# Optimization experiments

Hardware: AMD Instinct MI355X
Metric: run time of the kernel (lower is better)

## Reference

```python
import jax, jax.numpy as jnp
import numpy as np

CUTOFF_ENDS = [0, 20000, 40000, 200000, 267735]
D_EMBS = [1024, 256, 64, 16]
D_PROJ = 1024
EMB_SCALE = 1.0  # scale_emb=False


def setup_inputs() -> dict:
    key = jax.random.key(0)
    ks = jax.random.split(key, 9)
    out = {"inp": jax.random.randint(ks[0], (8, 2048), 0, CUTOFF_ENDS[-1], dtype=jnp.int64)
           if jax.config.jax_enable_x64 else
           jax.random.randint(ks[0], (8, 2048), 0, CUTOFF_ENDS[-1], dtype=jnp.int32)}
    for i in range(4):
        n_i = CUTOFF_ENDS[i + 1] - CUTOFF_ENDS[i]
        out[f"emb{i}"] = jax.random.normal(ks[1 + i], (n_i, D_EMBS[i]), jnp.float32) * 0.02
        out[f"proj{i}"] = jax.random.normal(ks[5 + i], (D_PROJ, D_EMBS[i]), jnp.float32) * 0.02
    return out


def reference(inp, emb0, emb1, emb2, emb3, proj0, proj1, proj2, proj3):
    # Faithful to AdaptiveEmbedding.forward: per-cutoff mask -> embedding lookup
    # -> linear projection (F.linear with weight [d_proj, d_emb_i]) -> scatter-back.
    # Instead of data-dependent nonzero/index_copy (not jit-able), each bucket
    # computes over all tokens with in-bucket indices clipped, then masked-adds;
    # disjoint buckets make this mathematically identical to the scatter.
    embs = [emb0, emb1, emb2, emb3]
    projs = [proj0, proj1, proj2, proj3]
    flat = inp.reshape(-1)                      # [N]
    out = jnp.zeros((flat.shape[0], D_PROJ), jnp.float32)
    for i in range(4):
        l, r = CUTOFF_ENDS[i], CUTOFF_ENDS[i + 1]
        mask = (flat >= l) & (flat < r)         # [N]
        idx = jnp.clip(flat - l, 0, r - l - 1)  # in-bucket ids, clipped for safety
        e = embs[i][idx]                        # [N, d_i] gather
        p = e @ projs[i].T                      # [N, d_proj] projection
        out = out + jnp.where(mask[:, None], p, 0.0)
    out = out.reshape(*inp.shape, D_PROJ)
    return out * EMB_SCALE if EMB_SCALE != 1.0 else out
```

## Files before the change

### kernel.cpp

```cpp
#include <hip/hip_runtime.h>

#define DPROJ 1024

typedef short  bf16x8 __attribute__((ext_vector_type(8)));
typedef float  f32x4  __attribute__((ext_vector_type(4)));
typedef unsigned short u16x4 __attribute__((ext_vector_type(4)));

__device__ __forceinline__ unsigned short f2bf(float f) {
  unsigned u = __builtin_bit_cast(unsigned, f);
  u += 0x7FFFu + ((u >> 16) & 1u);
  return (unsigned short)(u >> 16);
}

__device__ __forceinline__ int bucket_of(int v) {
  return (v < 0) ? -1 : (v >= 200000) ? 3 : (v >= 40000) ? 2 : (v >= 20000) ? 1 : 0;
}

__global__ __launch_bounds__(256) void count_kernel(const int* __restrict__ inp, int n,
                                                    int* __restrict__ blkcnt) {
  int t = blockIdx.x * 256 + threadIdx.x;
  int lane = threadIdx.x & 63, w = threadIdx.x >> 6;
  int v = (t < n) ? inp[t] : -1;
  int b = bucket_of(v);
  __shared__ int cnt[4][4];
#pragma unroll
  for (int i = 0; i < 4; ++i) {
    unsigned long long m = __ballot(b == i);
    if (lane == 0) cnt[w][i] = __popcll(m);
  }
  __syncthreads();
  if (threadIdx.x < 4) {
    int s = cnt[0][threadIdx.x] + cnt[1][threadIdx.x] +
            cnt[2][threadIdx.x] + cnt[3][threadIdx.x];
    blkcnt[blockIdx.x * 4 + threadIdx.x] = s;
  }
}

__global__ __launch_bounds__(256) void scatter_kernel(const int* __restrict__ inp, int n,
                                                      const int* __restrict__ blkcnt, int nb,
                                                      unsigned* __restrict__ lists,
                                                      int* __restrict__ counts) {
  int t = blockIdx.x * 256 + threadIdx.x;
  int lane = threadIdx.x & 63, w = threadIdx.x >> 6;
  __shared__ int cnt[4][4];
  __shared__ int off_s[4];
  {
    int sv = (lane < nb) ? blkcnt[lane * 4 + w] : 0;
    int x = sv;
#pragma unroll
    for (int d = 1; d < 64; d <<= 1) {
      int y = __shfl_up(x, d);
      if (lane >= d) x += y;
    }
    int myoff = __shfl(x - sv, blockIdx.x);
    if (lane == 0) off_s[w] = myoff;
    if (blockIdx.x == 0 && lane == 63) counts[w] = x;
  }
  int v = (t < n) ? inp[t] : -1;
  int b = bucket_of(v);
  int lo = (b == 3) ? 200000 : (b == 2) ? 40000 : (b == 1) ? 20000 : 0;
  int myrank = 0;
#pragma unroll
  for (int i = 0; i < 4; ++i) {
    unsigned long long m = __ballot(b == i);
    if (lane == 0) cnt[w][i] = __popcll(m);
    if (b == i) myrank = __popcll(m & ((1ull << lane) - 1ull));
  }
  __syncthreads();
  if (b >= 0) {
    int prefix = 0;
    for (int w2 = 0; w2 < w; ++w2) prefix += cnt[w2][b];
    int pos = off_s[b] + prefix + myrank;
    lists[(size_t)b * n + pos] = ((unsigned)(v - lo) << 14) | (unsigned)t;
  }
}

template <int D>
__device__ __forceinline__ void gemm_heavy(const float* __restrict__ emb,
                                           const float* __restrict__ proj,
                                           const unsigned* __restrict__ list,
                                           int cnt, int r0, int c0,
                                           float* __restrict__ out, char* smem) {
  constexpr int NCH = D / 64;
  const int tid  = threadIdx.x;
  const int lane = tid & 63;
  const int w    = tid >> 6;
  const int wr   = w >> 1, wc = w & 1;
  const int lr   = lane & 15, t16 = lane >> 4;

  char* Ab = smem;
  char* Bb = smem + 8192;
  unsigned* toks = (unsigned*)(smem + 24576);

  if (tid < 64) {
    int p = r0 + tid;
    toks[tid] = (p < cnt) ? list[p] : 0u;
  }
  __syncthreads();

  int ra[4], ca[4], cb[8], c4b[8];
#pragma unroll
  for (int i = 0; i < 4; ++i) {
    int q = tid + i * 256;
    ra[i] = q >> 4; ca[i] = (q & 15) * 4;
  }
#pragma unroll
  for (int i = 0; i < 8; ++i) {
    int q = tid + i * 256;
    cb[i] = q >> 4; c4b[i] = (q & 15) * 4;
  }
  const float* abase[4];
#pragma unroll
  for (int i = 0; i < 4; ++i)
    abase[i] = emb + (size_t)(toks[ra[i]] >> 14) * D + ca[i];
  const float* bbase[8];
#pragma unroll
  for (int i = 0; i < 8; ++i)
    bbase[i] = proj + (size_t)(c0 + cb[i]) * D + c4b[i];

  float4 arg[4], brg[8];
#pragma unroll
  for (int i = 0; i < 4; ++i) arg[i] = *reinterpret_cast<const float4*>(abase[i]);
#pragma unroll
  for (int i = 0; i < 8; ++i) brg[i] = *reinterpret_cast<const float4*>(bbase[i]);

  f32x4 acc[2][4];
#pragma unroll
  for (int fi = 0; fi < 2; ++fi)
#pragma unroll
    for (int fj = 0; fj < 4; ++fj) acc[fi][fj] = (f32x4){0.f, 0.f, 0.f, 0.f};

  for (int ch = 0; ch < NCH; ++ch) {
#pragma unroll
    for (int i = 0; i < 4; ++i) {
      u16x4 o = {f2bf(arg[i].x), f2bf(arg[i].y), f2bf(arg[i].z), f2bf(arg[i].w)};
      *reinterpret_cast<u16x4*>(Ab + ra[i] * 128 + ((ca[i] * 2) ^ ((ra[i] & 7) << 4))) = o;
    }
#pragma unroll
    for (int i = 0; i < 8; ++i) {
      u16x4 o = {f2bf(brg[i].x), f2bf(brg[i].y), f2bf(brg[i].z), f2bf(brg[i].w)};
      *reinterpret_cast<u16x4*>(Bb + cb[i] * 128 + ((c4b[i] * 2) ^ ((cb[i] & 7) << 4))) = o;
    }
    __syncthreads();

    if (ch + 1 < NCH) {
      const int k1 = (ch + 1) * 64;
#pragma unroll
      for (int i = 0; i < 4; ++i) arg[i] = *reinterpret_cast<const float4*>(abase[i] + k1);
#pragma unroll
      for (int i = 0; i < 8; ++i) brg[i] = *reinterpret_cast<const float4*>(bbase[i] + k1);
    }

#pragma unroll
    for (int s = 0; s < 2; ++s) {
      bf16x8 a[2], b[4];
#pragma unroll
      for (int fi = 0; fi < 2; ++fi) {
        int row = wr * 32 + fi * 16 + lr;
        a[fi] = *reinterpret_cast<const bf16x8*>(
            Ab + row * 128 + ((s * 64 + t16 * 16) ^ ((row & 7) << 4)));
      }
#pragma unroll
      for (int fj = 0; fj < 4; ++fj) {
        int col = wc * 64 + fj * 16 + lr;
        b[fj] = *reinterpret_cast<const bf16x8*>(
            Bb + col * 128 + ((s * 64 + t16 * 16) ^ ((col & 7) << 4)));
      }
#pragma unroll
      for (int fi = 0; fi < 2; ++fi)
#pragma unroll
        for (int fj = 0; fj < 4; ++fj)
          acc[fi][fj] = __builtin_amdgcn_mfma_f32_16x16x32_bf16(a[fi], b[fj], acc[fi][fj], 0, 0, 0);
    }
    __syncthreads();
  }

  float* T = reinterpret_cast<float*>(smem + w * 4352);
#pragma unroll
  for (int fi = 0; fi < 2; ++fi) {
#pragma unroll
    for (int fj = 0; fj < 4; ++fj)
#pragma unroll
      for (int reg = 0; reg < 4; ++reg)
        T[(t16 * 4 + reg) * 68 + fj * 16 + lr] = acc[fi][fj][reg];
#pragma unroll
    for (int rr = 0; rr < 4; ++rr) {
      int p = wr * 32 + fi * 16 + rr * 4 + t16;
      if (r0 + p < cnt) {
        float4 v = *reinterpret_cast<const float4*>(&T[(rr * 4 + t16) * 68 + lr * 4]);
        *reinterpret_cast<float4*>(out + (size_t)(toks[p] & 16383u) * DPROJ +
                                   c0 + wc * 64 + lr * 4) = v;
      }
    }
  }
}

template <int D>
__device__ __forceinline__ void gemm_light(const float* __restrict__ emb,
                                           const float* __restrict__ proj,
                                           const unsigned* __restrict__ list,
                                           int cnt, int r0, int c0,
                                           float* __restrict__ out, char* smem) {
  constexpr int S = (D == 64) ? 2 : 1;
  const int tid  = threadIdx.x;
  const int lane = tid & 63;
  const int w    = tid >> 6;
  const int wr   = w >> 1, wc = w & 1;
  const int lr   = lane & 15, t16 = lane >> 4;

  unsigned* toks = (unsigned*)smem;
  if (tid < 64) {
    int p = r0 + tid;
    toks[tid] = (p < cnt) ? list[p] : 0u;
  }
  __syncthreads();

  bf16x8 a[2][S], b[4][S];
#pragma unroll
  for (int fi = 0; fi < 2; ++fi) {
    const float* eb = emb + (size_t)(toks[wr * 32 + fi * 16 + lr] >> 14) * D;
#pragma unroll
    for (int s = 0; s < S; ++s) {
      float4 lo = make_float4(0.f, 0.f, 0.f, 0.f), hi = lo;
      if (D == 64 || t16 < 2) {
        lo = *reinterpret_cast<const float4*>(eb + s * 32 + t16 * 8);
        hi = *reinterpret_cast<const float4*>(eb + s * 32 + t16 * 8 + 4);
      }
      bf16x8 r;
      r[0] = (short)f2bf(lo.x); r[1] = (short)f2bf(lo.y);
      r[2] = (short)f2bf(lo.z); r[3] = (short)f2bf(lo.w);
      r[4] = (short)f2bf(hi.x); r[5] = (short)f2bf(hi.y);
      r[6] = (short)f2bf(hi.z); r[7] = (short)f2bf(hi.w);
      a[fi][s] = r;
    }
  }
#pragma unroll
  for (int fj = 0; fj < 4; ++fj) {
    const float* pb = proj + (size_t)(c0 + wc * 64 + fj * 16 + lr) * D;
#pragma unroll
    for (int s = 0; s < S; ++s) {
      float4 lo = make_float4(0.f, 0.f, 0.f, 0.f), hi = lo;
      if (D == 64 || t16 < 2) {
        lo = *reinterpret_cast<const float4*>(pb + s * 32 + t16 * 8);
        hi = *reinterpret_cast<const float4*>(pb + s * 32 + t16 * 8 + 4);
      }
      bf16x8 r;
      r[0] = (short)f2bf(lo.x); r[1] = (short)f2bf(lo.y);
      r[2] = (short)f2bf(lo.z); r[3] = (short)f2bf(lo.w);
      r[4] = (short)f2bf(hi.x); r[5] = (short)f2bf(hi.y);
      r[6] = (short)f2bf(hi.z); r[7] = (short)f2bf(hi.w);
      b[fj][s] = r;
    }
  }

  f32x4 acc[2][4];
#pragma unroll
  for (int fi = 0; fi < 2; ++fi)
#pragma unroll
    for (int fj = 0; fj < 4; ++fj) acc[fi][fj] = (f32x4){0.f, 0.f, 0.f, 0.f};
#pragma unroll
  for (int s = 0; s < S; ++s)
#pragma unroll
    for (int fi = 0; fi < 2; ++fi)
#pragma unroll
      for (int fj = 0; fj < 4; ++fj)
        acc[fi][fj] = __builtin_amdgcn_mfma_f32_16x16x32_bf16(a[fi][s], b[fj][s], acc[fi][fj], 0, 0, 0);

  float* T = reinterpret_cast<float*>(smem + 256) + w * 1088;
#pragma unroll
  for (int fi = 0; fi < 2; ++fi) {
#pragma unroll
    for (int fj = 0; fj < 4; ++fj)
#pragma unroll
      for (int reg = 0; reg < 4; ++reg)
        T[(t16 * 4 + reg) * 68 + fj * 16 + lr] = acc[fi][fj][reg];
#pragma unroll
    for (int rr = 0; rr < 4; ++rr) {
      int p = wr * 32 + fi * 16 + rr * 4 + t16;
      if (r0 + p < cnt) {
        float4 v = *reinterpret_cast<const float4*>(&T[(rr * 4 + t16) * 68 + lr * 4]);
        *reinterpret_cast<float4*>(out + (size_t)(toks[p] & 16383u) * DPROJ +
                                   c0 + wc * 64 + lr * 4) = v;
      }
    }
  }
}

__global__ __launch_bounds__(256) void gemm_all(
    const float* __restrict__ e0, const float* __restrict__ p0,
    const float* __restrict__ e1, const float* __restrict__ p1,
    const float* __restrict__ e2, const float* __restrict__ p2,
    const float* __restrict__ e3, const float* __restrict__ p3,
    const int* __restrict__ counts, const unsigned* __restrict__ lists,
    float* __restrict__ out, int n) {
  extern __shared__ char smem[];
  int bx = blockIdx.x;
  int t  = bx >> 3;
  int c0 = (bx & 7) * 128;
  int4 c = *reinterpret_cast<const int4*>(counts);
  int t0 = (c.x + 63) >> 6, t1 = (c.y + 63) >> 6,
      t2 = (c.z + 63) >> 6, t3 = (c.w + 63) >> 6;
  if (t < t0) { gemm_heavy<1024>(e0, p0, lists,               c.x, t * 64, c0, out, smem); return; }
  t -= t0;
  if (t < t1) { gemm_heavy< 256>(e1, p1, lists + (size_t)n,   c.y, t * 64, c0, out, smem); return; }
  t -= t1;
  if (t < t2) { gemm_light<64>(e2, p2, lists + (size_t)2 * n, c.z, t * 64, c0, out, smem); return; }
  t -= t2;
  if (t < t3) { gemm_light<16>(e3, p3, lists + (size_t)3 * n, c.w, t * 64, c0, out, smem); return; }
}

extern "C" void kernel_launch(void* const* d_in, const int* in_sizes, int n_in,
                              void* d_out, int out_size, void* d_ws, size_t ws_size,
                              hipStream_t stream) {
  const int*   inp   = (const int*)d_in[0];
  const float* emb0  = (const float*)d_in[1];
  const float* proj0 = (const float*)d_in[2];
  const float* emb1  = (const float*)d_in[3];
  const float* proj1 = (const float*)d_in[4];
  const float* emb2  = (const float*)d_in[5];
  const float* proj2 = (const float*)d_in[6];
  const float* emb3  = (const float*)d_in[7];
  const float* proj3 = (const float*)d_in[8];
  float* out = (float*)d_out;
  const int n = in_sizes[0];

  int*      counts = (int*)d_ws;
  int*      blkcnt = (int*)d_ws + 4;
  unsigned* lists  = (unsigned*)d_ws + 260;

  const int nb = (n + 255) / 256;
  count_kernel<<<dim3(nb), dim3(256), 0, stream>>>(inp, n, blkcnt);
  scatter_kernel<<<dim3(nb), dim3(256), 0, stream>>>(inp, n, blkcnt, nb, lists, counts);

  dim3 grid(259 * 8, 1, 1);
  size_t smem_bytes = 24576 + 64 * sizeof(unsigned);
  gemm_all<<<grid, dim3(256), smem_bytes, stream>>>(emb0, proj0, emb1, proj1,
                                                    emb2, proj2, emb3, proj3,
                                                    counts, lists, out, n);
}
```

Baseline: 43.82 us.

## Pre-convert projections to bf16, split-K the heavy bucket, double-buffer loads

Adds a pre-pass that converts all projection matrices to bf16 in workspace, fused with the bucket counting kernel, so GEMM blocks read half-width B tiles without per-block conversion. The heavy bucket 0 (D=1024) is split four ways along K for up to `cap` tiles. Each split writes partials to workspace, and a new reduce kernel sums them and scatters rows into the output. The heavy GEMM loop is fully unrolled with two register sets of prefetched loads. The goal is better load balance, since bucket-0 blocks were long-running stragglers, and lower conversion cost. The price is an extra launch, partial-sum memory traffic, a projection conversion on every call, and higher register pressure.

```diff
diff --git a/kernel.cpp b/kernel.cpp
--- a/kernel.cpp
+++ b/kernel.cpp
@@ -4,7 +4,6 @@
 
 typedef short  bf16x8 __attribute__((ext_vector_type(8)));
 typedef float  f32x4  __attribute__((ext_vector_type(4)));
-typedef unsigned short u16x4 __attribute__((ext_vector_type(4)));
 
 __device__ __forceinline__ unsigned short f2bf(float f) {
   unsigned u = __builtin_bit_cast(unsigned, f);
@@ -12,27 +11,52 @@
   return (unsigned short)(u >> 16);
 }
 
+__device__ __forceinline__ bf16x8 pack8(float4 lo, float4 hi) {
+  bf16x8 r;
+  r[0] = (short)f2bf(lo.x); r[1] = (short)f2bf(lo.y);
+  r[2] = (short)f2bf(lo.z); r[3] = (short)f2bf(lo.w);
+  r[4] = (short)f2bf(hi.x); r[5] = (short)f2bf(hi.y);
+  r[6] = (short)f2bf(hi.z); r[7] = (short)f2bf(hi.w);
+  return r;
+}
+
 __device__ __forceinline__ int bucket_of(int v) {
-  return (v < 0) ? -1 : (v >= 200000) ? 3 : (v >= 40000) ? 2 : (v >= 20000) ? 1 : 0;
-}
-
-__global__ __launch_bounds__(256) void count_kernel(const int* __restrict__ inp, int n,
-                                                    int* __restrict__ blkcnt) {
-  int t = blockIdx.x * 256 + threadIdx.x;
-  int lane = threadIdx.x & 63, w = threadIdx.x >> 6;
-  int v = (t < n) ? inp[t] : -1;
-  int b = bucket_of(v);
-  __shared__ int cnt[4][4];
-#pragma unroll
-  for (int i = 0; i < 4; ++i) {
-    unsigned long long m = __ballot(b == i);
-    if (lane == 0) cnt[w][i] = __popcll(m);
-  }
-  __syncthreads();
-  if (threadIdx.x < 4) {
-    int s = cnt[0][threadIdx.x] + cnt[1][threadIdx.x] +
-            cnt[2][threadIdx.x] + cnt[3][threadIdx.x];
-    blkcnt[blockIdx.x * 4 + threadIdx.x] = s;
+  return (v >= 200000) ? 3 : (v >= 40000) ? 2 : (v >= 20000) ? 1 : 0;
+}
+
+__global__ __launch_bounds__(256) void convert_count(
+    const float* __restrict__ p0, const float* __restrict__ p1,
+    const float* __restrict__ p2, const float* __restrict__ p3,
+    unsigned short* __restrict__ pb,
+    const int* __restrict__ inp, int n, int nb, int* __restrict__ blkcnt) {
+  size_t base = ((size_t)blockIdx.x * 256 + threadIdx.x) * 8;
+  if (base < 1392640u) {
+    const float* src;
+    if      (base < 1048576u) src = p0 + base;
+    else if (base < 1310720u) src = p1 + (base - 1048576u);
+    else if (base < 1376256u) src = p2 + (base - 1310720u);
+    else                      src = p3 + (base - 1376256u);
+    float4 lo = reinterpret_cast<const float4*>(src)[0];
+    float4 hi = reinterpret_cast<const float4*>(src)[1];
+    *reinterpret_cast<bf16x8*>(pb + base) = pack8(lo, hi);
+  }
+  if (blockIdx.x < (unsigned)nb) {
+    int t = blockIdx.x * 256 + threadIdx.x;
+    int lane = threadIdx.x & 63, w = threadIdx.x >> 6;
+    int v = (t < n) ? inp[t] : -1;
+    int b = (v < 0) ? -1 : bucket_of(v);
+    __shared__ int cnt[4][4];
+#pragma unroll
+    for (int i = 0; i < 4; ++i) {
+      unsigned long long m = __ballot(b == i);
+      if (lane == 0) cnt[w][i] = __popcll(m);
+    }
+    __syncthreads();
+    if (threadIdx.x < 4) {
+      int s = cnt[0][threadIdx.x] + cnt[1][threadIdx.x] +
+              cnt[2][threadIdx.x] + cnt[3][threadIdx.x];
+      blkcnt[blockIdx.x * 4 + threadIdx.x] = s;
+    }
   }
 }
 
@@ -57,7 +81,7 @@
     if (blockIdx.x == 0 && lane == 63) counts[w] = x;
   }
   int v = (t < n) ? inp[t] : -1;
-  int b = bucket_of(v);
+  int b = (v < 0) ? -1 : bucket_of(v);
   int lo = (b == 3) ? 200000 : (b == 2) ? 40000 : (b == 1) ? 20000 : 0;
   int myrank = 0;
 #pragma unroll
@@ -75,13 +99,12 @@
   }
 }
 
-template <int D>
+template <int D, int CHB, bool PARTIAL>
 __device__ __forceinline__ void gemm_heavy(const float* __restrict__ emb,
-                                           const float* __restrict__ proj,
+                                           const unsigned short* __restrict__ pbD,
                                            const unsigned* __restrict__ list,
-                                           int cnt, int r0, int c0,
-                                           float* __restrict__ out, char* smem) {
-  constexpr int NCH = D / 64;
+                                           int cnt, int r0, int c0, int ch0,
+                                           float* __restrict__ dst, char* smem) {
   const int tid  = threadIdx.x;
   const int lane = tid & 63;
   const int w    = tid >> 6;
@@ -98,31 +121,43 @@
   }
   __syncthreads();
 
-  int ra[4], ca[4], cb[8], c4b[8];
+  int rowA[2], kkA[2], colB[4], kkB[4];
+#pragma unroll
+  for (int i = 0; i < 2; ++i) {
+    int g = tid + i * 256;
+    rowA[i] = g >> 3; kkA[i] = (g & 7) * 8;
+  }
 #pragma unroll
   for (int i = 0; i < 4; ++i) {
-    int q = tid + i * 256;
-    ra[i] = q >> 4; ca[i] = (q & 15) * 4;
-  }
-#pragma unroll
-  for (int i = 0; i < 8; ++i) {
-    int q = tid + i * 256;
-    cb[i] = q >> 4; c4b[i] = (q & 15) * 4;
-  }
-  const float* abase[4];
+    int g = tid + i * 256;
+    colB[i] = g >> 3; kkB[i] = (g & 7) * 8;
+  }
+  const float* abase[2];
+#pragma unroll
+  for (int i = 0; i < 2; ++i)
+    abase[i] = emb + (size_t)(toks[rowA[i]] >> 14) * D + kkA[i];
+  const unsigned short* bbase[4];
 #pragma unroll
   for (int i = 0; i < 4; ++i)
-    abase[i] = emb + (size_t)(toks[ra[i]] >> 14) * D + ca[i];
-  const float* bbase[8];
-#pragma unroll
-  for (int i = 0; i < 8; ++i)
-    bbase[i] = proj + (size_t)(c0 + cb[i]) * D + c4b[i];
-
-  float4 arg[4], brg[8];
-#pragma unroll
-  for (int i = 0; i < 4; ++i) arg[i] = *reinterpret_cast<const float4*>(abase[i]);
-#pragma unroll
-  for (int i = 0; i < 8; ++i) brg[i] = *reinterpret_cast<const float4*>(bbase[i]);
+    bbase[i] = pbD + (size_t)(c0 + colB[i]) * D + kkB[i];
+
+  float4  arg[2][2][2];
+  bf16x8  brg[2][4];
+
+#define LOAD_SET(S_, K0_)                                                   \
+  {                                                                         \
+    _Pragma("unroll")                                                       \
+    for (int i = 0; i < 2; ++i) {                                           \
+      arg[S_][i][0] = *reinterpret_cast<const float4*>(abase[i] + (K0_));   \
+      arg[S_][i][1] = *reinterpret_cast<const float4*>(abase[i] + (K0_) + 4);\
+    }                                                                       \
+    _Pragma("unroll")                                                       \
+    for (int i = 0; i < 4; ++i)                                             \
+      brg[S_][i] = *reinterpret_cast<const bf16x8*>(bbase[i] + (K0_));      \
+  }
+
+  LOAD_SET(0, ch0 * 64)
+  if (CHB > 1) LOAD_SET(1, (ch0 + 1) * 64)
 
   f32x4 acc[2][4];
 #pragma unroll
@@ -130,26 +165,22 @@
 #pragma unroll
     for (int fj = 0; fj < 4; ++fj) acc[fi][fj] = (f32x4){0.f, 0.f, 0.f, 0.f};
 
-  for (int ch = 0; ch < NCH; ++ch) {
-#pragma unroll
-    for (int i = 0; i < 4; ++i) {
-      u16x4 o = {f2bf(arg[i].x), f2bf(arg[i].y), f2bf(arg[i].z), f2bf(arg[i].w)};
-      *reinterpret_cast<u16x4*>(Ab + ra[i] * 128 + ((ca[i] * 2) ^ ((ra[i] & 7) << 4))) = o;
-    }
-#pragma unroll
-    for (int i = 0; i < 8; ++i) {
-      u16x4 o = {f2bf(brg[i].x), f2bf(brg[i].y), f2bf(brg[i].z), f2bf(brg[i].w)};
-      *reinterpret_cast<u16x4*>(Bb + cb[i] * 128 + ((c4b[i] * 2) ^ ((cb[i] & 7) << 4))) = o;
-    }
+#pragma unroll
+  for (int ch = 0; ch < CHB; ++ch) {
+    const int cur = ch & 1;
+#pragma unroll
+    for (int i = 0; i < 2; ++i) {
+      bf16x8 o = pack8(arg[cur][i][0], arg[cur][i][1]);
+      *reinterpret_cast<bf16x8*>(Ab + rowA[i] * 128 +
+                                 ((kkA[i] * 2) ^ ((rowA[i] & 7) << 4))) = o;
+    }
+#pragma unroll
+    for (int i = 0; i < 4; ++i)
+      *reinterpret_cast<bf16x8*>(Bb + colB[i] * 128 +
+                                 ((kkB[i] * 2) ^ ((colB[i] & 7) << 4))) = brg[cur][i];
     __syncthreads();
 
-    if (ch + 1 < NCH) {
-      const int k1 = (ch + 1) * 64;
-#pragma unroll
-      for (int i = 0; i < 4; ++i) arg[i] = *reinterpret_cast<const float4*>(abase[i] + k1);
-#pragma unroll
-      for (int i = 0; i < 8; ++i) brg[i] = *reinterpret_cast<const float4*>(bbase[i] + k1);
-    }
+    if (ch + 2 < CHB) LOAD_SET(cur, (ch0 + ch + 2) * 64)
 
 #pragma unroll
     for (int s = 0; s < 2; ++s) {
@@ -174,6 +205,7 @@
     }
     __syncthreads();
   }
+#undef LOAD_SET
 
   float* T = reinterpret_cast<float*>(smem + w * 4352);
 #pragma unroll
@@ -188,8 +220,11 @@
       int p = wr * 32 + fi * 16 + rr * 4 + t16;
       if (r0 + p < cnt) {
         float4 v = *reinterpret_cast<const float4*>(&T[(rr * 4 + t16) * 68 + lr * 4]);
-        *reinterpret_cast<float4*>(out + (size_t)(toks[p] & 16383u) * DPROJ +
-                                   c0 + wc * 64 + lr * 4) = v;
+        if (PARTIAL)
+          *reinterpret_cast<float4*>(dst + (size_t)p * 128 + wc * 64 + lr * 4) = v;
+        else
+          *reinterpret_cast<float4*>(dst + (size_t)(toks[p] & 16383u) * DPROJ +
+                                     c0 + wc * 64 + lr * 4) = v;
       }
     }
   }
@@ -197,7 +232,7 @@
 
 template <int D>
 __device__ __forceinline__ void gemm_light(const float* __restrict__ emb,
-                                           const float* __restrict__ proj,
+                                           const unsigned short* __restrict__ pbD,
                                            const unsigned* __restrict__ list,
                                            int cnt, int r0, int c0,
                                            float* __restrict__ out, char* smem) {
@@ -226,30 +261,18 @@
         lo = *reinterpret_cast<const float4*>(eb + s * 32 + t16 * 8);
         hi = *reinterpret_cast<const float4*>(eb + s * 32 + t16 * 8 + 4);
       }
-      bf16x8 r;
-      r[0] = (short)f2bf(lo.x); r[1] = (short)f2bf(lo.y);
-      r[2] = (short)f2bf(lo.z); r[3] = (short)f2bf(lo.w);
-      r[4] = (short)f2bf(hi.x); r[5] = (short)f2bf(hi.y);
-      r[6] = (short)f2bf(hi.z); r[7] = (short)f2bf(hi.w);
-      a[fi][s] = r;
+      a[fi][s] = pack8(lo, hi);
     }
   }
 #pragma unroll
   for (int fj = 0; fj < 4; ++fj) {
-    const float* pb = proj + (size_t)(c0 + wc * 64 + fj * 16 + lr) * D;
+    const unsigned short* pbc = pbD + (size_t)(c0 + wc * 64 + fj * 16 + lr) * D;
 #pragma unroll
     for (int s = 0; s < S; ++s) {
-      float4 lo = make_float4(0.f, 0.f, 0.f, 0.f), hi = lo;
-      if (D == 64 || t16 < 2) {
-        lo = *reinterpret_cast<const float4*>(pb + s * 32 + t16 * 8);
-        hi = *reinterpret_cast<const float4*>(pb + s * 32 + t16 * 8 + 4);
-      }
-      bf16x8 r;
-      r[0] = (short)f2bf(lo.x); r[1] = (short)f2bf(lo.y);
-      r[2] = (short)f2bf(lo.z); r[3] = (short)f2bf(lo.w);
-      r[4] = (short)f2bf(hi.x); r[5] = (short)f2bf(hi.y);
-      r[6] = (short)f2bf(hi.z); r[7] = (short)f2bf(hi.w);
-      b[fj][s] = r;
+      bf16x8 z = {0, 0, 0, 0, 0, 0, 0, 0};
+      if (D == 64 || t16 < 2)
+        z = *reinterpret_cast<const bf16x8*>(pbc + s * 32 + t16 * 8);
+      b[fj][s] = z;
     }
   }
 
@@ -287,26 +310,82 @@
 }
 
 __global__ __launch_bounds__(256) void gemm_all(
-    const float* __restrict__ e0, const float* __restrict__ p0,
-    const float* __restrict__ e1, const float* __restrict__ p1,
-    const float* __restrict__ e2, const float* __restrict__ p2,
-    const float* __restrict__ e3, const float* __restrict__ p3,
+    const float* __restrict__ e0, const float* __restrict__ e1,
+    const float* __restrict__ e2, const float* __restrict__ e3,
+    const unsigned short* __restrict__ pb,
     const int* __restrict__ counts, const unsigned* __restrict__ lists,
-    float* __restrict__ out, int n) {
+    float* __restrict__ part, float* __restrict__ out, int n, int cap) {
   extern __shared__ char smem[];
-  int bx = blockIdx.x;
-  int t  = bx >> 3;
-  int c0 = (bx & 7) * 128;
   int4 c = *reinterpret_cast<const int4*>(counts);
   int t0 = (c.x + 63) >> 6, t1 = (c.y + 63) >> 6,
       t2 = (c.z + 63) >> 6, t3 = (c.w + 63) >> 6;
-  if (t < t0) { gemm_heavy<1024>(e0, p0, lists,               c.x, t * 64, c0, out, smem); return; }
-  t -= t0;
-  if (t < t1) { gemm_heavy< 256>(e1, p1, lists + (size_t)n,   c.y, t * 64, c0, out, smem); return; }
-  t -= t1;
-  if (t < t2) { gemm_light<64>(e2, p2, lists + (size_t)2 * n, c.z, t * 64, c0, out, smem); return; }
-  t -= t2;
-  if (t < t3) { gemm_light<16>(e3, p3, lists + (size_t)3 * n, c.w, t * 64, c0, out, smem); return; }
+  int sk = (t0 < cap) ? t0 : cap;
+  int y = blockIdx.x;
+  if (y < sk * 32) {
+    int nb0 = sk * 8;
+    int kz = y / nb0, r = y % nb0;
+    int tile = r >> 3, slice = r & 7;
+    float* dst = part + ((size_t)(r * 4 + kz)) * 8192;
+    gemm_heavy<1024, 4, true>(e0, pb, lists, c.x, tile * 64, slice * 128,
+                              kz * 4, dst, smem);
+    return;
+  }
+  y -= sk * 32;
+  if (y < (t0 - sk) * 8) {
+    int tile = sk + (y >> 3), slice = y & 7;
+    gemm_heavy<1024, 16, false>(e0, pb, lists, c.x, tile * 64, slice * 128,
+                                0, out, smem);
+    return;
+  }
+  y -= (t0 - sk) * 8;
+  if (y < t1 * 8) {
+    gemm_heavy<256, 4, false>(e1, pb + 1048576, lists + (size_t)n, c.y,
+                              (y >> 3) * 64, (y & 7) * 128, 0, out, smem);
+    return;
+  }
+  y -= t1 * 8;
+  if (y < t2 * 8) {
+    gemm_light<64>(e2, pb + 1310720, lists + (size_t)2 * n, c.z,
+                   (y >> 3) * 64, (y & 7) * 128, out, smem);
+    return;
+  }
+  y -= t2 * 8;
+  if (y < t3 * 8) {
+    gemm_light<16>(e3, pb + 1376256, lists + (size_t)3 * n, c.w,
+                   (y >> 3) * 64, (y & 7) * 128, out, smem);
+    return;
+  }
+}
+
+__global__ __launch_bounds__(256) void reduce_b0(const int* __restrict__ counts,
+                                                 const unsigned* __restrict__ list0,
+                                                 const float* __restrict__ part,
+                                                 float* __restrict__ out, int cap) {
+  int cnt = counts[0];
+  int tiles = (cnt + 63) >> 6;
+  if (tiles > cap) tiles = cap;
+  int tile = blockIdx.y, slice = blockIdx.x;
+  if (tile >= tiles) return;
+  const float* base = part + ((size_t)((tile * 8 + slice) * 4)) * 8192;
+  int tid = threadIdx.x;
+  int r0 = tile * 64;
+#pragma unroll
+  for (int pass = 0; pass < 8; ++pass) {
+    int row = pass * 8 + (tid >> 5);
+    int p = r0 + row;
+    if (p < cnt) {
+      int off = row * 128 + (tid & 31) * 4;
+      float4 v0 = *reinterpret_cast<const float4*>(base + off);
+      float4 v1 = *reinterpret_cast<const float4*>(base + 8192 + off);
+      float4 v2 = *reinterpret_cast<const float4*>(base + 16384 + off);
+      float4 v3 = *reinterpret_cast<const float4*>(base + 24576 + off);
+      float4 s = make_float4(v0.x + v1.x + v2.x + v3.x, v0.y + v1.y + v2.y + v3.y,
+                             v0.z + v1.z + v2.z + v3.z, v0.w + v1.w + v2.w + v3.w);
+      unsigned tok = list0[p] & 16383u;
+      *reinterpret_cast<float4*>(out + (size_t)tok * DPROJ + slice * 128 +
+                                 (tid & 31) * 4) = s;
+    }
+  }
 }
 
 extern "C" void kernel_launch(void* const* d_in, const int* in_sizes, int n_in,
@@ -324,17 +403,28 @@
   float* out = (float*)d_out;
   const int n = in_sizes[0];
 
-  int*      counts = (int*)d_ws;
-  int*      blkcnt = (int*)d_ws + 4;
-  unsigned* lists  = (unsigned*)d_ws + 260;
+  int*            counts = (int*)d_ws;
+  int*            blkcnt = (int*)d_ws + 4;
+  unsigned*       lists  = (unsigned*)d_ws + 260;
+  unsigned short* pb     = (unsigned short*)((char*)d_ws + 524288);
+  const size_t    PART_OFF = 3309568;
+  const size_t    PER_TILE = 8u * 4u * 8192u * 4u;
+  int cap = 0;
+  if (ws_size > PART_OFF) {
+    size_t cc = (ws_size - PART_OFF) / PER_TILE;
+    cap = (cc > 32) ? 32 : (int)cc;
+  }
+  float* part = (float*)((char*)d_ws + PART_OFF);
 
   const int nb = (n + 255) / 256;
-  count_kernel<<<dim3(nb), dim3(256), 0, stream>>>(inp, n, blkcnt);
+  convert_count<<<dim3(680), dim3(256), 0, stream>>>(proj0, proj1, proj2, proj3,
+                                                     pb, inp, n, nb, blkcnt);
   scatter_kernel<<<dim3(nb), dim3(256), 0, stream>>>(inp, n, blkcnt, nb, lists, counts);
 
-  dim3 grid(259 * 8, 1, 1);
+  dim3 grid(cap * 32 + ((n + 63) / 64 + 3) * 8, 1, 1);
   size_t smem_bytes = 24576 + 64 * sizeof(unsigned);
-  gemm_all<<<grid, dim3(256), smem_bytes, stream>>>(emb0, proj0, emb1, proj1,
-                                                    emb2, proj2, emb3, proj3,
-                                                    counts, lists, out, n);
-}
+  gemm_all<<<grid, dim3(256), smem_bytes, stream>>>(emb0, emb1, emb2, emb3, pb,
+                                                    counts, lists, part, out, n, cap);
+  if (cap > 0)
+    reduce_b0<<<dim3(8, cap), dim3(256), 0, stream>>>(counts, lists, part, out, cap);
+}
```

Result: slower. 46.03 us (+5.0%).
